# Optimization experiments

Hardware: AMD Instinct MI355X
Metric: run time of the kernel (lower is better)

The kernel has to match this reference:

```python
import jax, jax.numpy as jnp
import numpy as np

GRID_SIZE = 8
POS_LAMBDA = 250.0
POS_MARGIN = 1.0
NEG_MARGIN = 0.2


def setup_inputs() -> dict:
    key = jax.random.key(0)
    k1, k2, k3, k4 = jax.random.split(key, 4)
    N, C, Hr, Wr = 8, 128, 30, 40
    H, W = Hr * GRID_SIZE, Wr * GRID_SIZE
    des1 = jax.random.normal(k1, (N, C, Hr, Wr), jnp.float32)
    des2 = jax.random.normal(k2, (N, C, Hr, Wr), jnp.float32)
    # near-identity homography so the positive-pair mask s is non-trivial
    homo = jnp.eye(3, dtype=jnp.float32) + 0.001 * jax.random.normal(k3, (3, 3), jnp.float32)
    mask = (jax.random.uniform(k4, (N, 1, H, W)) > 0.05).astype(jnp.float32)
    return {"des1": des1, "des2": des2, "homo": homo, "mask": mask}


def reference(des1, des2, homo, mask):
    n, c, hr, wr = des1.shape
    gs = GRID_SIZE

    # coordinate grid of cell centers in full-res pixel coords: (x, y)
    ys, xs = jnp.meshgrid(jnp.arange(hr), jnp.arange(wr), indexing='ij')
    grid = jnp.stack([xs, ys], axis=-1).astype(homo.dtype) * gs + gs // 2  # Hr,Wr,2
    grid = jnp.broadcast_to(grid, (n, hr, wr, 2))

    # warp grid by homography
    gh = jnp.concatenate([grid, jnp.ones((n, hr, wr, 1), homo.dtype)], axis=-1)  # N,Hr,Wr,3
    wg = jnp.einsum('nhwk,jk->nhwj', gh, homo)
    w_grid = wg[..., :2] / wg[..., 2:3]  # N,Hr,Wr,2

    # pairwise distance between grid cells of img1 and warped cells of img2
    diff = grid[:, :, :, None, None, :] - w_grid[:, None, None, :, :, :]  # N,Hr,Wr,Hr,Wr,2
    grid_dist = jnp.sqrt(jnp.sum(diff * diff, axis=-1))                   # N,Hr,Wr,Hr,Wr
    s = (grid_dist <= gs - 0.5).astype(des1.dtype)

    # dense descriptor cross-correlation (contraction over channels)
    dot_des = jnp.einsum('ncij,nckl->nijkl', des1, des2)  # N,Hr,Wr,Hr,Wr

    pos_dist = jnp.maximum(POS_MARGIN - dot_des, 0.0)
    neg_dist = jnp.maximum(dot_des - NEG_MARGIN, 0.0)
    loss = POS_LAMBDA * s * pos_dist + (1.0 - s) * neg_dist

    # space_to_depth(mask, gs).prod(dim=1)
    m = mask.reshape(n, 1, hr, gs, wr, gs)
    r_mask = jnp.prod(m, axis=(1, 3, 5))            # N,Hr,Wr
    r_mask5 = r_mask.reshape(n, 1, 1, hr, wr)

    norm = hr * wr * jnp.sum(r_mask5)
    loss = jnp.sum(loss * r_mask5) / norm
    return (loss, s, dot_des, r_mask5[:, 0])  # r_mask squeezed -> N,1,Hr,Wr
```

## Files before the change

### kernel.cpp

```cpp
#include <hip/hip_runtime.h>
#include <hip/hip_bf16.h>

#define HRr 30
#define WRr 40
#define MM 1200
#define CC 128
#define NB 8
#define GS 8

constexpr int BM = 64, BN = 64;
constexpr int PT = (MM + BM - 1) / BM;
constexpr int NPART = NB * PT * PT;
constexpr int TILE_SH = 16 * 64 * 8;

typedef __attribute__((ext_vector_type(8))) short bf16x8;
typedef __attribute__((ext_vector_type(4))) float f32x4;

__device__ inline short f2bf(float f) {
    union { float f; unsigned u; } v; v.f = f;
    unsigned r = v.u + 0x7FFFu + ((v.u >> 16) & 1u);
    return (short)(r >> 16);
}

__global__ __launch_bounds__(256) void convert_prep_kernel(const float* __restrict__ des1,
                                                           const float* __restrict__ des2,
                                                           const float* __restrict__ homo,
                                                           const float* __restrict__ mask,
                                                           short* __restrict__ wsA,
                                                           short* __restrict__ wsB,
                                                           float2* __restrict__ wgrid,
                                                           float* __restrict__ out_rmask,
                                                           float* __restrict__ ws_rmask) {
    const int t     = threadIdx.x;
    const int ptile = blockIdx.x;
    const int n     = blockIdx.z;

    const int gid = (blockIdx.z * gridDim.x + blockIdx.x) * 256 + t;
    if (gid < MM) {
        int k = gid / WRr, l = gid % WRr;
        float x = (float)(l * GS + GS / 2);
        float y = (float)(k * GS + GS / 2);
        float nx = homo[0] * x + homo[1] * y + homo[2];
        float ny = homo[3] * x + homo[4] * y + homo[5];
        float dn = homo[6] * x + homo[7] * y + homo[8];
        wgrid[gid] = make_float2(nx / dn, ny / dn);
    }
    if (gid < NB * MM) {
        int nn = gid / MM;
        int rem = gid % MM;
        int k = rem / WRr, l = rem % WRr;
        const float* mp = mask + (size_t)nn * (240 * 320) + (size_t)(k * GS) * 320 + l * GS;
        float prod = 1.f;
        #pragma unroll
        for (int yy = 0; yy < GS; ++yy) {
            float4 a = *reinterpret_cast<const float4*>(&mp[yy * 320]);
            float4 b = *reinterpret_cast<const float4*>(&mp[yy * 320 + 4]);
            prod *= a.x * a.y * a.z * a.w * b.x * b.y * b.z * b.w;
        }
        out_rmask[gid] = prod;
        ws_rmask[gid]  = prod;
    }

    const int j = t & 63;
    const int g = t >> 6;
    const int p = ptile * BM + j;

    const float* A = des1 + (size_t)n * CC * MM;
    const float* B = des2 + (size_t)n * CC * MM;
    short* outA = wsA + (size_t)(n * PT + ptile) * TILE_SH;
    short* outB = wsB + (size_t)(n * PT + ptile) * TILE_SH;

    const int rb = j >> 4, lc = j & 15;
    #pragma unroll
    for (int it = 0; it < 4; ++it) {
        const int kr = it * 4 + g;
        const int kb = kr * 8;
        bf16x8 wa, wb;
        #pragma unroll
        for (int i = 0; i < 8; ++i) {
            float va = (p < MM) ? A[(size_t)(kb + i) * MM + p] : 0.f;
            float vb = (p < MM) ? B[(size_t)(kb + i) * MM + p] : 0.f;
            wa[i] = f2bf(va);
            wb[i] = f2bf(vb);
        }
        const int ks = kr >> 2, lr = kr & 3;
        const size_t off = (size_t)(((ks * 4 + rb) * 64) + lr * 16 + lc) * 8;
        *reinterpret_cast<bf16x8*>(&outA[off]) = wa;
        *reinterpret_cast<bf16x8*>(&outB[off]) = wb;
    }
}

__global__ __launch_bounds__(256) void main_kernel(const short* __restrict__ wsA,
                                                   const short* __restrict__ wsB,
                                                   const float2* __restrict__ wgrid,
                                                   const float* __restrict__ rmask,
                                                   float* __restrict__ out_s,
                                                   float* __restrict__ out_dot,
                                                   float* __restrict__ partials) {
    __shared__ float Ds[64 * 68];
    __shared__ float red[4];

    const int n  = blockIdx.z;
    const int p0 = blockIdx.y * BM;
    const int q0 = blockIdx.x * BN;
    const int t  = threadIdx.x;
    const int l  = t & 63;
    const int lr = l >> 4;
    const int lc = l & 15;
    const int w  = t >> 6;
    const int wrow = (w >> 1) * 32;
    const int wcol = (w & 1) * 32;

    const short* Abase = wsA + (size_t)(n * PT + blockIdx.y) * TILE_SH;
    const short* Bbase = wsB + (size_t)(n * PT + blockIdx.x) * TILE_SH;

    f32x4 acc[2][2] = {};
    #pragma unroll
    for (int ks = 0; ks < 4; ++ks) {
        bf16x8 af[2], bfr[2];
        #pragma unroll
        for (int f = 0; f < 2; ++f) {
            const int rbA = (w >> 1) * 2 + f;
            const int rbB = (w & 1) * 2 + f;
            af[f]  = *reinterpret_cast<const bf16x8*>(&Abase[(size_t)(((ks * 4 + rbA) * 64) + l) * 8]);
            bfr[f] = *reinterpret_cast<const bf16x8*>(&Bbase[(size_t)(((ks * 4 + rbB) * 64) + l) * 8]);
        }
        #pragma unroll
        for (int fi = 0; fi < 2; ++fi)
            #pragma unroll
            for (int fj = 0; fj < 2; ++fj)
                acc[fi][fj] = __builtin_amdgcn_mfma_f32_16x16x32_bf16(af[fi], bfr[fj], acc[fi][fj], 0, 0, 0);
    }

    #pragma unroll
    for (int fi = 0; fi < 2; ++fi)
        #pragma unroll
        for (int fj = 0; fj < 2; ++fj)
            #pragma unroll
            for (int rr = 0; rr < 4; ++rr)
                Ds[(wrow + fi * 16 + lr * 4 + rr) * 68 + wcol + fj * 16 + lc] = acc[fi][fj][rr];
    __syncthreads();

    float lsum = 0.f;
    #pragma unroll
    for (int r = 0; r < 16; ++r) {
        const int idx = r * 256 + t;
        const int row = idx >> 6;
        const int col = idx & 63;
        const int pp = p0 + row;
        const int qq = q0 + col;
        if (pp < MM) {
            const float gx = (float)((pp % WRr) * GS + GS / 2);
            const float gy = (float)((pp / WRr) * GS + GS / 2);
            const float dot = Ds[row * 68 + col];
            if (qq < MM) {
                const float2 wg = wgrid[qq];
                const float dx = gx - wg.x;
                const float dy = gy - wg.y;
                const float dist = sqrtf(dx * dx + dy * dy);
                const float s = (dist <= (float)GS - 0.5f) ? 1.f : 0.f;
                const float pos = fmaxf(1.f - dot, 0.f);
                const float neg = fmaxf(dot - 0.2f, 0.f);
                const float le = 250.f * s * pos + (1.f - s) * neg;
                lsum += le * rmask[n * MM + qq];
                const size_t gidx = ((size_t)(n * MM + pp)) * MM + qq;
                out_dot[gidx] = dot;
                out_s[gidx] = s;
            }
        }
    }

    #pragma unroll
    for (int off = 32; off > 0; off >>= 1)
        lsum += __shfl_xor(lsum, off, 64);
    if (l == 0) red[w] = lsum;
    __syncthreads();
    if (t == 0)
        partials[(size_t)blockIdx.z * (PT * PT) + blockIdx.y * PT + blockIdx.x] =
            (red[0] + red[1]) + (red[2] + red[3]);
}

__global__ __launch_bounds__(1024) void final_kernel(const float* __restrict__ partials,
                                                     const float* __restrict__ rmask,
                                                     float* __restrict__ out_loss) {
    __shared__ float red[1024];
    const int t = threadIdx.x;

    float s1 = 0.f;
    for (int i = t; i < NPART; i += 1024) s1 += partials[i];
    red[t] = s1;
    __syncthreads();
    for (int off = 512; off > 0; off >>= 1) {
        if (t < off) red[t] += red[t + off];
        __syncthreads();
    }
    float total = red[0];
    __syncthreads();

    float s2 = 0.f;
    for (int i = t; i < NB * MM; i += 1024) s2 += rmask[i];
    red[t] = s2;
    __syncthreads();
    for (int off = 512; off > 0; off >>= 1) {
        if (t < off) red[t] += red[t + off];
        __syncthreads();
    }
    if (t == 0) out_loss[0] = total / ((float)MM * red[0]);
}

extern "C" void kernel_launch(void* const* d_in, const int* in_sizes, int n_in,
                              void* d_out, int out_size, void* d_ws, size_t ws_size,
                              hipStream_t stream) {
    const float* des1 = (const float*)d_in[0];
    const float* des2 = (const float*)d_in[1];
    const float* homo = (const float*)d_in[2];
    const float* mask = (const float*)d_in[3];

    float* out      = (float*)d_out;
    float* out_loss = out;
    float* out_s    = out + 1;
    float* out_dot  = out + 1 + (size_t)NB * MM * MM;
    float* out_rm   = out + 1 + 2 * (size_t)NB * MM * MM;

    char* wsb = (char*)d_ws;
    float2* wgrid    = (float2*)(wsb);
    float*  partials = (float*)(wsb + 16384);
    float*  ws_rm    = (float*)(wsb + 32768);
    short*  wsA      = (short*)(wsb + 131072);
    short*  wsB      = wsA + (size_t)NB * PT * TILE_SH;

    dim3 cgrid(PT, 1, NB);
    convert_prep_kernel<<<cgrid, 256, 0, stream>>>(des1, des2, homo, mask,
                                                   wsA, wsB, wgrid, out_rm, ws_rm);

    dim3 grid(PT, PT, NB);
    main_kernel<<<grid, 256, 0, stream>>>(wsA, wsB, wgrid, ws_rm, out_s, out_dot, partials);

    final_kernel<<<1, 1024, 0, stream>>>(partials, ws_rm, out_loss);
}
```

Before: 48.13 us.

## Restructure main kernel into 16-row strips spanning full output rows with vectorized stores

Each block now handles a 16-row strip of one batch across all 1200 columns, processed in two passes. The A fragments are held in registers and reused across every column tile. The epilogue writes contiguous row segments with aligned float4 stores for dot and s, with scalar head and tail loops to handle alignment. This replaces 64x64 tiles whose 256-byte row segments gave poorly coalesced stores. The block-to-index mapping interleaves batches across the grid, and fewer, larger blocks (600) may lower occupancy and load balance.

```diff
diff --git a/kernel.cpp b/kernel.cpp
--- a/kernel.cpp
+++ b/kernel.cpp
@@ -8,10 +8,10 @@
 #define NB 8
 #define GS 8
 
-constexpr int BM = 64, BN = 64;
-constexpr int PT = (MM + BM - 1) / BM;
-constexpr int NPART = NB * PT * PT;
+constexpr int PT = 19;
 constexpr int TILE_SH = 16 * 64 * 8;
+constexpr int NSTRIP = 75;
+constexpr int NPART = NB * NSTRIP;
 
 typedef __attribute__((ext_vector_type(8))) short bf16x8;
 typedef __attribute__((ext_vector_type(4))) float f32x4;
@@ -63,7 +63,7 @@
 
     const int j = t & 63;
     const int g = t >> 6;
-    const int p = ptile * BM + j;
+    const int p = ptile * 64 + j;
 
     const float* A = des1 + (size_t)n * CC * MM;
     const float* B = des2 + (size_t)n * CC * MM;
@@ -97,87 +97,122 @@
                                                    float* __restrict__ out_s,
                                                    float* __restrict__ out_dot,
                                                    float* __restrict__ partials) {
-    __shared__ float Ds[64 * 68];
+    __shared__ float Ds[16 * 612];
     __shared__ float red[4];
 
-    const int n  = blockIdx.z;
-    const int p0 = blockIdx.y * BM;
-    const int q0 = blockIdx.x * BN;
-    const int t  = threadIdx.x;
-    const int l  = t & 63;
-    const int lr = l >> 4;
-    const int lc = l & 15;
-    const int w  = t >> 6;
-    const int wrow = (w >> 1) * 32;
-    const int wcol = (w & 1) * 32;
-
-    const short* Abase = wsA + (size_t)(n * PT + blockIdx.y) * TILE_SH;
-    const short* Bbase = wsB + (size_t)(n * PT + blockIdx.x) * TILE_SH;
-
-    f32x4 acc[2][2] = {};
-    #pragma unroll
-    for (int ks = 0; ks < 4; ++ks) {
-        bf16x8 af[2], bfr[2];
-        #pragma unroll
-        for (int f = 0; f < 2; ++f) {
-            const int rbA = (w >> 1) * 2 + f;
-            const int rbB = (w & 1) * 2 + f;
-            af[f]  = *reinterpret_cast<const bf16x8*>(&Abase[(size_t)(((ks * 4 + rbA) * 64) + l) * 8]);
-            bfr[f] = *reinterpret_cast<const bf16x8*>(&Bbase[(size_t)(((ks * 4 + rbB) * 64) + l) * 8]);
-        }
-        #pragma unroll
-        for (int fi = 0; fi < 2; ++fi)
+    const int f   = blockIdx.x;
+    const int lid = (f & 7) * NSTRIP + (f >> 3);
+    const int n     = lid / NSTRIP;
+    const int strip = lid % NSTRIP;
+    const int p0 = strip * 16;
+
+    const int t    = threadIdx.x;
+    const int lane = t & 63;
+    const int w    = t >> 6;
+    const int lr   = lane >> 4, lc = lane & 15;
+
+    const short* An  = wsA + (size_t)(n * PT + (p0 >> 6)) * TILE_SH;
+    const int    rbA = (p0 >> 4) & 3;
+    bf16x8 af[4];
+    #pragma unroll
+    for (int ks = 0; ks < 4; ++ks)
+        af[ks] = *reinterpret_cast<const bf16x8*>(&An[(size_t)(((ks * 4 + rbA) * 64) + lane) * 8]);
+
+    const short* Bn = wsB + (size_t)n * PT * TILE_SH;
+    const float* rm = rmask + n * MM;
+
+    const int row = t >> 4;
+    const int l16 = t & 15;
+    const int p   = p0 + row;
+    const float gx = (float)((p % WRr) * GS + GS / 2);
+    const float gy = (float)((p / WRr) * GS + GS / 2);
+    const size_t rowbase = (size_t)(n * MM + p) * MM;
+    const int h = 31 - 16 * (p & 1);
+
+    float lsum = 0.f;
+
+    #pragma unroll
+    for (int pass = 0; pass < 2; ++pass) {
+        const int cbase = pass ? 608 : 0;
+        const int nf    = pass ? 37  : 38;
+        const int W     = pass ? 592 : 608;
+
+        for (int i = w; i < nf; i += 4) {
+            const int g = (cbase >> 4) + i;
+            const short* Bt = Bn + (size_t)(g >> 2) * TILE_SH;
+            const int rbB = g & 3;
+            f32x4 acc = {0.f, 0.f, 0.f, 0.f};
             #pragma unroll
-            for (int fj = 0; fj < 2; ++fj)
-                acc[fi][fj] = __builtin_amdgcn_mfma_f32_16x16x32_bf16(af[fi], bfr[fj], acc[fi][fj], 0, 0, 0);
-    }
-
-    #pragma unroll
-    for (int fi = 0; fi < 2; ++fi)
-        #pragma unroll
-        for (int fj = 0; fj < 2; ++fj)
+            for (int ks = 0; ks < 4; ++ks) {
+                bf16x8 bfr = *reinterpret_cast<const bf16x8*>(
+                    &Bt[(size_t)(((ks * 4 + rbB) * 64) + lane) * 8]);
+                acc = __builtin_amdgcn_mfma_f32_16x16x32_bf16(af[ks], bfr, acc, 0, 0, 0);
+            }
             #pragma unroll
-            for (int rr = 0; rr < 4; ++rr)
-                Ds[(wrow + fi * 16 + lr * 4 + rr) * 68 + wcol + fj * 16 + lc] = acc[fi][fj][rr];
-    __syncthreads();
-
-    float lsum = 0.f;
-    #pragma unroll
-    for (int r = 0; r < 16; ++r) {
-        const int idx = r * 256 + t;
-        const int row = idx >> 6;
-        const int col = idx & 63;
-        const int pp = p0 + row;
-        const int qq = q0 + col;
-        if (pp < MM) {
-            const float gx = (float)((pp % WRr) * GS + GS / 2);
-            const float gy = (float)((pp / WRr) * GS + GS / 2);
-            const float dot = Ds[row * 68 + col];
-            if (qq < MM) {
-                const float2 wg = wgrid[qq];
-                const float dx = gx - wg.x;
-                const float dy = gy - wg.y;
+            for (int r = 0; r < 4; ++r)
+                Ds[(lr * 4 + r) * 612 + 1 + i * 16 + lc] = acc[r];
+        }
+        __syncthreads();
+
+        const int nl = (W - h) >> 5;
+        const int s4 = nl << 3;
+        const int ts = h + (nl << 5);
+
+        for (int c = l16; c < h; c += 16) {
+            const float dot = Ds[row * 612 + 1 + c];
+            const int q = cbase + c;
+            const float2 wg = wgrid[q];
+            const float dx = gx - wg.x, dy = gy - wg.y;
+            const float dist = sqrtf(dx * dx + dy * dy);
+            const float s = (dist <= 7.5f) ? 1.f : 0.f;
+            const float le = 250.f * s * fmaxf(1.f - dot, 0.f) + (1.f - s) * fmaxf(dot - 0.2f, 0.f);
+            lsum += le * rm[q];
+            out_dot[rowbase + q] = dot;
+            out_s[rowbase + q] = s;
+        }
+        for (int k = 0;; ++k) {
+            const int jj = l16 + (k << 4);
+            if (jj >= s4) break;
+            const int c = h + (jj << 2);
+            const int q = cbase + c;
+            const float4 dv = *reinterpret_cast<const float4*>(&Ds[row * 612 + 1 + c]);
+            float sv[4];
+            const float dd[4] = {dv.x, dv.y, dv.z, dv.w};
+            #pragma unroll
+            for (int u = 0; u < 4; ++u) {
+                const float2 wg = wgrid[q + u];
+                const float dx = gx - wg.x, dy = gy - wg.y;
                 const float dist = sqrtf(dx * dx + dy * dy);
-                const float s = (dist <= (float)GS - 0.5f) ? 1.f : 0.f;
-                const float pos = fmaxf(1.f - dot, 0.f);
-                const float neg = fmaxf(dot - 0.2f, 0.f);
-                const float le = 250.f * s * pos + (1.f - s) * neg;
-                lsum += le * rmask[n * MM + qq];
-                const size_t gidx = ((size_t)(n * MM + pp)) * MM + qq;
-                out_dot[gidx] = dot;
-                out_s[gidx] = s;
+                const float s = (dist <= 7.5f) ? 1.f : 0.f;
+                sv[u] = s;
+                const float le = 250.f * s * fmaxf(1.f - dd[u], 0.f) + (1.f - s) * fmaxf(dd[u] - 0.2f, 0.f);
+                lsum += le * rm[q + u];
             }
-        }
+            *reinterpret_cast<float4*>(&out_dot[rowbase + q]) = dv;
+            *reinterpret_cast<float4*>(&out_s[rowbase + q]) = make_float4(sv[0], sv[1], sv[2], sv[3]);
+        }
+        for (int c = ts + l16; c < W; c += 16) {
+            const float dot = Ds[row * 612 + 1 + c];
+            const int q = cbase + c;
+            const float2 wg = wgrid[q];
+            const float dx = gx - wg.x, dy = gy - wg.y;
+            const float dist = sqrtf(dx * dx + dy * dy);
+            const float s = (dist <= 7.5f) ? 1.f : 0.f;
+            const float le = 250.f * s * fmaxf(1.f - dot, 0.f) + (1.f - s) * fmaxf(dot - 0.2f, 0.f);
+            lsum += le * rm[q];
+            out_dot[rowbase + q] = dot;
+            out_s[rowbase + q] = s;
+        }
+        __syncthreads();
     }
 
     #pragma unroll
     for (int off = 32; off > 0; off >>= 1)
         lsum += __shfl_xor(lsum, off, 64);
-    if (l == 0) red[w] = lsum;
+    if (lane == 0) red[w] = lsum;
     __syncthreads();
     if (t == 0)
-        partials[(size_t)blockIdx.z * (PT * PT) + blockIdx.y * PT + blockIdx.x] =
-            (red[0] + red[1]) + (red[2] + red[3]);
+        partials[lid] = (red[0] + red[1]) + (red[2] + red[3]);
 }
 
 __global__ __launch_bounds__(1024) void final_kernel(const float* __restrict__ partials,
@@ -233,8 +268,8 @@
     convert_prep_kernel<<<cgrid, 256, 0, stream>>>(des1, des2, homo, mask,
                                                    wsA, wsB, wgrid, out_rm, ws_rm);
 
-    dim3 grid(PT, PT, NB);
-    main_kernel<<<grid, 256, 0, stream>>>(wsA, wsB, wgrid, ws_rm, out_s, out_dot, partials);
+    main_kernel<<<dim3(NPART, 1, 1), 256, 0, stream>>>(wsA, wsB, wgrid, ws_rm,
+                                                       out_s, out_dot, partials);
 
     final_kernel<<<1, 1024, 0, stream>>>(partials, ws_rm, out_loss);
 }
```

New measurement: 50.19 us. 4.3% more time.
